# Optimization experiments

Hardware: AMD Instinct MI355X
Metric: run time of the kernel (lower is better)

## Reference

```python
import jax, jax.numpy as jnp
import numpy as np

IOU_POS = 0.5
IOU_NEG = 0.3


def _pairwise_iou(b1, b2):
    # b1: [N,4], b2: [M,4] in xyxy -> [N,M]
    area1 = (b1[:, 2] - b1[:, 0]) * (b1[:, 3] - b1[:, 1])
    area2 = (b2[:, 2] - b2[:, 0]) * (b2[:, 3] - b2[:, 1])
    lt = jnp.maximum(b1[:, None, :2], b2[None, :, :2])
    rb = jnp.minimum(b1[:, None, 2:], b2[None, :, 2:])
    wh = jnp.clip(rb - lt, 0.0)
    inter = wh[..., 0] * wh[..., 1]
    union = area1[:, None] + area2[None, :] - inter
    return inter / jnp.maximum(union, 1e-8)


def _smooth_l1(x):
    ax = jnp.abs(x)
    return jnp.where(ax < 1.0, 0.5 * x * x, ax - 0.5)


def _per_image(cls_o, reg_o, tb, tl):
    # cls_o: [N,C], reg_o: [N,4], tb: [M,4], tl: [M]
    ious = _pairwise_iou(reg_o, tb)            # [N,M]
    max_ious = ious.max(axis=1)
    max_idx = ious.argmax(axis=1)
    pos = max_ious >= IOU_POS
    neg = max_ious < IOU_NEG
    logp = jax.nn.log_softmax(cls_o, axis=-1)  # [N,C]
    matched_lbl = tl[max_idx]                  # [N]
    ce_pos = -jnp.take_along_axis(logp, matched_lbl[:, None], axis=1)[:, 0]
    ce_neg = -logp[:, 0]                       # background class 0
    npos = pos.sum().astype(logp.dtype)
    nneg = neg.sum().astype(logp.dtype)
    cls_loss_pos = jnp.sum(jnp.where(pos, ce_pos, 0.0)) / jnp.maximum(npos, 1.0)
    cls_loss_neg = jnp.sum(jnp.where(neg, ce_neg, 0.0)) / jnp.maximum(nneg, 1.0)
    diff = reg_o - tb[max_idx]                 # [N,4]
    sl1 = _smooth_l1(diff).mean(axis=-1)       # per-anchor mean over 4 coords
    reg_loss = jnp.sum(jnp.where(pos, sl1, 0.0)) / jnp.maximum(npos, 1.0)
    return cls_loss_pos, cls_loss_neg, reg_loss, npos > 0, nneg > 0


def _detection_loss(cls_output, reg_output, target_boxes, target_labels):
    cp, cn, rl, has_p, has_n = jax.vmap(_per_image)(cls_output, reg_output, target_boxes, target_labels)
    cls_vals = jnp.concatenate([cp, cn])
    cls_valid = jnp.concatenate([has_p, has_n]).astype(cls_vals.dtype)
    n_cls = cls_valid.sum()
    cls_mean = jnp.sum(cls_vals * cls_valid) / jnp.maximum(n_cls, 1.0)
    has_pf = has_p.astype(rl.dtype)
    n_reg = has_pf.sum()
    reg_mean = jnp.sum(rl * has_pf) / jnp.maximum(n_reg, 1.0)
    total = jnp.where(n_cls > 0, cls_mean, 0.0) + jnp.where(n_reg > 0, reg_mean, 0.0)
    return total


def setup_inputs() -> dict:
    key = jax.random.key(0)
    k1, k2, k3, k4, k5, k6 = jax.random.split(key, 6)
    B, N, C, M = 8, 131072, 21, 32
    cls_output = jax.random.normal(k1, (B, N, C), dtype=jnp.float32)
    xy = jax.random.uniform(k2, (B, N, 2), minval=0.0, maxval=220.0)
    wh = jax.random.uniform(k3, (B, N, 2), minval=20.0, maxval=80.0)
    reg_output = jnp.concatenate([xy, xy + wh], axis=-1)
    txy = jax.random.uniform(k4, (B, M, 2), minval=0.0, maxval=220.0)
    twh = jax.random.uniform(k5, (B, M, 2), minval=20.0, maxval=80.0)
    target_boxes = jnp.concatenate([txy, txy + twh], axis=-1)
    target_labels = jax.random.randint(k6, (B, M), 1, C)
    return {"cls_output": cls_output, "reg_output": reg_output,
            "target_boxes": target_boxes, "target_labels": target_labels}


def reference(cls_output, reg_output, target_boxes, target_labels):
    return _detection_loss(cls_output, reg_output, target_boxes, target_labels)
```

## Files before the change

### kernel.cpp

```cpp
#include <hip/hip_runtime.h>
#include <math.h>

#define TPB 256
#define TPB4 4
#define NC 21
#define NM 32

__global__ __launch_bounds__(TPB) void detloss_main(
    const float* __restrict__ cls, const float* __restrict__ reg,
    const float* __restrict__ tbx, const int* __restrict__ tlb,
    float* __restrict__ partials, int N, int gxb)
{
    __shared__ float s_red[TPB / 64][5];

    const int t    = threadIdx.x;
    const int lane = t & 63;
    const int w    = t >> 6;
    const int blk  = blockIdx.x;
    const int b    = blockIdx.y;
    const int ntiles = (N + TPB - 1) / TPB;
    const int tile0  = blk * TPB4;
    const int tile1  = min(tile0 + TPB4, ntiles);

    float v0 = 0.f, v1 = 0.f, v2 = 0.f, v3 = 0.f, v4 = 0.f;

    for (int tile = tile0; tile < tile1; ++tile) {
        const int row  = tile * TPB + t;
        const int rowi = (row < N) ? row : (N - 1);
        const float msk = (row < N) ? 1.f : 0.f;

        const float4 rg = ((const float4*)reg)[(size_t)b * N + rowi];
        const float a1 = (rg.z - rg.x) * (rg.w - rg.y);

        const char* xg = (const char*)(cls + ((size_t)b * N + rowi) * NC);
        float4 c0, c1, c2, c3, c4; float c5;
        __builtin_memcpy(&c0, xg,      16);
        __builtin_memcpy(&c1, xg + 16, 16);
        __builtin_memcpy(&c2, xg + 32, 16);
        __builtin_memcpy(&c3, xg + 48, 16);
        __builtin_memcpy(&c4, xg + 64, 16);
        __builtin_memcpy(&c5, xg + 80, 4);

        unsigned kbest = 0u;
        #pragma unroll
        for (int j = 0; j < NM; ++j) {
            const float4 tb = ((const float4*)tbx)[b * NM + j];
            const float ta = (tb.z - tb.x) * (tb.w - tb.y);
            const float lx = fmaxf(rg.x, tb.x), ly = fmaxf(rg.y, tb.y);
            const float rx = fminf(rg.z, tb.z), ry = fminf(rg.w, tb.w);
            const float wd = fmaxf(rx - lx, 0.f), h = fmaxf(ry - ly, 0.f);
            const float inter = wd * h;
            const float uni   = (a1 + ta) - inter;
            const float iou   = inter * __builtin_amdgcn_rcpf(uni);
            const unsigned key = (__float_as_uint(iou) & 0xFFFFFFE0u)
                               | (unsigned)(31 - j);
            kbest = (key > kbest) ? key : kbest;
        }
        const int   bidx = 31 - (int)(kbest & 31u);
        const float best = __uint_as_float(kbest & 0xFFFFFFE0u);
        const bool  pos  = (best >= 0.5f);
        const bool  neg  = (best <  0.3f);

        const int    lbl = tlb[b * NM + bidx];
        const float4 mb  = ((const float4*)tbx)[b * NM + bidx];
        float xlbl;
        __builtin_memcpy(&xlbl, xg + 4 * lbl, 4);

        float s0 = __expf(c0.x) + __expf(c0.y) + __expf(c0.z) + __expf(c0.w);
        float s1 = __expf(c1.x) + __expf(c1.y) + __expf(c1.z) + __expf(c1.w);
        float s2 = __expf(c2.x) + __expf(c2.y) + __expf(c2.z) + __expf(c2.w);
        float s3 = __expf(c3.x) + __expf(c3.y) + __expf(c3.z) + __expf(c3.w);
        s0 += __expf(c4.x) + __expf(c4.y);
        s1 += __expf(c4.z) + __expf(c4.w);
        s2 += __expf(c5);
        const float lse    = __logf((s0 + s1) + (s2 + s3));
        const float ce_pos = lse - xlbl;
        const float ce_neg = lse - c0.x;

        float sl = 0.f;
        {
            const float d0 = rg.x - mb.x, d1 = rg.y - mb.y;
            const float d2 = rg.z - mb.z, d3 = rg.w - mb.w;
            const float e0 = fabsf(d0), e1 = fabsf(d1);
            const float e2 = fabsf(d2), e3 = fabsf(d3);
            sl += (e0 < 1.f) ? 0.5f * d0 * d0 : (e0 - 0.5f);
            sl += (e1 < 1.f) ? 0.5f * d1 * d1 : (e1 - 0.5f);
            sl += (e2 < 1.f) ? 0.5f * d2 * d2 : (e2 - 0.5f);
            sl += (e3 < 1.f) ? 0.5f * d3 * d3 : (e3 - 0.5f);
            sl *= 0.25f;
        }

        const float pm = (pos ? 1.f : 0.f) * msk;
        const float nm = (neg ? 1.f : 0.f) * msk;
        v0 += pm * ce_pos; v2 += pm * sl; v3 += pm;
        v1 += nm * ce_neg; v4 += nm;
    }

    #pragma unroll
    for (int o = 32; o > 0; o >>= 1) {
        v0 += __shfl_down(v0, o);
        v1 += __shfl_down(v1, o);
        v2 += __shfl_down(v2, o);
        v3 += __shfl_down(v3, o);
        v4 += __shfl_down(v4, o);
    }
    if (lane == 0) {
        s_red[w][0] = v0; s_red[w][1] = v1; s_red[w][2] = v2;
        s_red[w][3] = v3; s_red[w][4] = v4;
    }
    __syncthreads();
    if (t == 0) {
        float r0 = 0, r1 = 0, r2 = 0, r3 = 0, r4 = 0;
        #pragma unroll
        for (int k = 0; k < TPB / 64; ++k) {
            r0 += s_red[k][0]; r1 += s_red[k][1]; r2 += s_red[k][2];
            r3 += s_red[k][3]; r4 += s_red[k][4];
        }
        float* q = partials + ((size_t)b * gxb + blk) * 5;
        q[0] = r0; q[1] = r1; q[2] = r2; q[3] = r3; q[4] = r4;
    }
}

__global__ __launch_bounds__(512) void detloss_final(
    const float* __restrict__ partials, int nblk, int B, float* __restrict__ out)
{
    __shared__ float s_img[8][5];
    const int t    = threadIdx.x;
    const int b    = t >> 6;
    const int lane = t & 63;

    if (b < B) {
        float v[5] = {0.f, 0.f, 0.f, 0.f, 0.f};
        for (int e = lane; e < nblk; e += 64) {
            const float* q = partials + ((size_t)b * nblk + e) * 5;
            #pragma unroll
            for (int k = 0; k < 5; ++k) v[k] += q[k];
        }
        #pragma unroll
        for (int o = 32; o > 0; o >>= 1) {
            #pragma unroll
            for (int k = 0; k < 5; ++k) v[k] += __shfl_down(v[k], o);
        }
        if (lane == 0) {
            const float npos = v[3], nneg = v[4];
            s_img[b][0] = v[0] / fmaxf(npos, 1.f);
            s_img[b][1] = v[1] / fmaxf(nneg, 1.f);
            s_img[b][2] = v[2] / fmaxf(npos, 1.f);
            s_img[b][3] = (npos > 0.f) ? 1.f : 0.f;
            s_img[b][4] = (nneg > 0.f) ? 1.f : 0.f;
        }
    }
    __syncthreads();

    if (t == 0) {
        float cls_sum = 0.f, n_cls = 0.f, reg_sum = 0.f, n_reg = 0.f;
        for (int b2 = 0; b2 < B; ++b2) {
            cls_sum += s_img[b2][0] * s_img[b2][3] + s_img[b2][1] * s_img[b2][4];
            n_cls   += s_img[b2][3] + s_img[b2][4];
            reg_sum += s_img[b2][2] * s_img[b2][3];
            n_reg   += s_img[b2][3];
        }
        const float cls_mean = cls_sum / fmaxf(n_cls, 1.f);
        const float reg_mean = reg_sum / fmaxf(n_reg, 1.f);
        out[0] = ((n_cls > 0.f) ? cls_mean : 0.f) + ((n_reg > 0.f) ? reg_mean : 0.f);
    }
}

extern "C" void kernel_launch(void* const* d_in, const int* in_sizes, int n_in,
                              void* d_out, int out_size, void* d_ws, size_t ws_size,
                              hipStream_t stream) {
    const float* cls = (const float*)d_in[0];
    const float* reg = (const float*)d_in[1];
    const float* tbx = (const float*)d_in[2];
    const int*   tlb = (const int*)d_in[3];
    float*       out = (float*)d_out;
    float*  partials = (float*)d_ws;

    const int B = 8;
    const int N = in_sizes[1] / (B * 4);
    const int ntiles = (N + TPB - 1) / TPB;
    const int gxb    = (ntiles + TPB4 - 1) / TPB4;

    dim3 grid(gxb, B);
    detloss_main<<<grid, TPB, 0, stream>>>(cls, reg, tbx, tlb, partials, N, gxb);
    detloss_final<<<1, 512, 0, stream>>>(partials, gxb, B, out);
}
```

Before: 40.74 us.

## Use one-wavefront blocks with one row per thread and no LDS reduction

The main kernel now launches 64-thread blocks, each thread handling exactly one anchor row. This replaces 256-thread blocks that looped over four tiles. The shared-memory cross-wave reduction and its barrier are removed, so each block writes its wavefront-reduced partials directly with a vector store. The aim is more independent loads in flight and less per-block synchronisation. In exchange the partials array grows 16-fold, and the single-block final kernel must sum many more strided entries.

```diff
diff --git a/kernel.cpp b/kernel.cpp
--- a/kernel.cpp
+++ b/kernel.cpp
@@ -1,100 +1,87 @@
 #include <hip/hip_runtime.h>
 #include <math.h>
 
-#define TPB 256
-#define TPB4 4
+#define WPB 64
 #define NC 21
 #define NM 32
 
-__global__ __launch_bounds__(TPB) void detloss_main(
+__global__ __launch_bounds__(WPB) void detloss_main(
     const float* __restrict__ cls, const float* __restrict__ reg,
     const float* __restrict__ tbx, const int* __restrict__ tlb,
-    float* __restrict__ partials, int N, int gxb)
+    float* __restrict__ partials, int N, int nblk)
 {
-    __shared__ float s_red[TPB / 64][5];
+    const int t   = threadIdx.x;
+    const int blk = blockIdx.x;
+    const int b   = blockIdx.y;
+    const int row = blk * WPB + t;
+    const int rowi = (row < N) ? row : (N - 1);
+    const float msk = (row < N) ? 1.f : 0.f;
 
-    const int t    = threadIdx.x;
-    const int lane = t & 63;
-    const int w    = t >> 6;
-    const int blk  = blockIdx.x;
-    const int b    = blockIdx.y;
-    const int ntiles = (N + TPB - 1) / TPB;
-    const int tile0  = blk * TPB4;
-    const int tile1  = min(tile0 + TPB4, ntiles);
+    const float4 rg = ((const float4*)reg)[(size_t)b * N + rowi];
+    const float a1 = (rg.z - rg.x) * (rg.w - rg.y);
 
-    float v0 = 0.f, v1 = 0.f, v2 = 0.f, v3 = 0.f, v4 = 0.f;
+    const char* xg = (const char*)(cls + ((size_t)b * N + rowi) * NC);
+    float4 c0, c1, c2, c3, c4; float c5;
+    __builtin_memcpy(&c0, xg,      16);
+    __builtin_memcpy(&c1, xg + 16, 16);
+    __builtin_memcpy(&c2, xg + 32, 16);
+    __builtin_memcpy(&c3, xg + 48, 16);
+    __builtin_memcpy(&c4, xg + 64, 16);
+    __builtin_memcpy(&c5, xg + 80, 4);
 
-    for (int tile = tile0; tile < tile1; ++tile) {
-        const int row  = tile * TPB + t;
-        const int rowi = (row < N) ? row : (N - 1);
-        const float msk = (row < N) ? 1.f : 0.f;
+    unsigned kbest = 0u;
+    #pragma unroll
+    for (int j = 0; j < NM; ++j) {
+        const float4 tb = ((const float4*)tbx)[b * NM + j];
+        const float ta = (tb.z - tb.x) * (tb.w - tb.y);
+        const float lx = fmaxf(rg.x, tb.x), ly = fmaxf(rg.y, tb.y);
+        const float rx = fminf(rg.z, tb.z), ry = fminf(rg.w, tb.w);
+        const float wd = fmaxf(rx - lx, 0.f), h = fmaxf(ry - ly, 0.f);
+        const float inter = wd * h;
+        const float uni   = (a1 + ta) - inter;
+        const float iou   = inter * __builtin_amdgcn_rcpf(uni);
+        const unsigned key = (__float_as_uint(iou) & 0xFFFFFFE0u)
+                           | (unsigned)(31 - j);
+        kbest = (key > kbest) ? key : kbest;
+    }
+    const int   bidx = 31 - (int)(kbest & 31u);
+    const float best = __uint_as_float(kbest & 0xFFFFFFE0u);
+    const bool  pos  = (best >= 0.5f);
+    const bool  neg  = (best <  0.3f);
 
-        const float4 rg = ((const float4*)reg)[(size_t)b * N + rowi];
-        const float a1 = (rg.z - rg.x) * (rg.w - rg.y);
+    const int    lbl = tlb[b * NM + bidx];
+    const float4 mb  = ((const float4*)tbx)[b * NM + bidx];
+    float xlbl;
+    __builtin_memcpy(&xlbl, xg + 4 * lbl, 4);
 
-        const char* xg = (const char*)(cls + ((size_t)b * N + rowi) * NC);
-        float4 c0, c1, c2, c3, c4; float c5;
-        __builtin_memcpy(&c0, xg,      16);
-        __builtin_memcpy(&c1, xg + 16, 16);
-        __builtin_memcpy(&c2, xg + 32, 16);
-        __builtin_memcpy(&c3, xg + 48, 16);
-        __builtin_memcpy(&c4, xg + 64, 16);
-        __builtin_memcpy(&c5, xg + 80, 4);
+    float s0 = __expf(c0.x) + __expf(c0.y) + __expf(c0.z) + __expf(c0.w);
+    float s1 = __expf(c1.x) + __expf(c1.y) + __expf(c1.z) + __expf(c1.w);
+    float s2 = __expf(c2.x) + __expf(c2.y) + __expf(c2.z) + __expf(c2.w);
+    float s3 = __expf(c3.x) + __expf(c3.y) + __expf(c3.z) + __expf(c3.w);
+    s0 += __expf(c4.x) + __expf(c4.y);
+    s1 += __expf(c4.z) + __expf(c4.w);
+    s2 += __expf(c5);
+    const float lse    = __logf((s0 + s1) + (s2 + s3));
+    const float ce_pos = lse - xlbl;
+    const float ce_neg = lse - c0.x;
 
-        unsigned kbest = 0u;
-        #pragma unroll
-        for (int j = 0; j < NM; ++j) {
-            const float4 tb = ((const float4*)tbx)[b * NM + j];
-            const float ta = (tb.z - tb.x) * (tb.w - tb.y);
-            const float lx = fmaxf(rg.x, tb.x), ly = fmaxf(rg.y, tb.y);
-            const float rx = fminf(rg.z, tb.z), ry = fminf(rg.w, tb.w);
-            const float wd = fmaxf(rx - lx, 0.f), h = fmaxf(ry - ly, 0.f);
-            const float inter = wd * h;
-            const float uni   = (a1 + ta) - inter;
-            const float iou   = inter * __builtin_amdgcn_rcpf(uni);
-            const unsigned key = (__float_as_uint(iou) & 0xFFFFFFE0u)
-                               | (unsigned)(31 - j);
-            kbest = (key > kbest) ? key : kbest;
-        }
-        const int   bidx = 31 - (int)(kbest & 31u);
-        const float best = __uint_as_float(kbest & 0xFFFFFFE0u);
-        const bool  pos  = (best >= 0.5f);
-        const bool  neg  = (best <  0.3f);
+    float sl = 0.f;
+    {
+        const float d0 = rg.x - mb.x, d1 = rg.y - mb.y;
+        const float d2 = rg.z - mb.z, d3 = rg.w - mb.w;
+        const float e0 = fabsf(d0), e1 = fabsf(d1);
+        const float e2 = fabsf(d2), e3 = fabsf(d3);
+        sl += (e0 < 1.f) ? 0.5f * d0 * d0 : (e0 - 0.5f);
+        sl += (e1 < 1.f) ? 0.5f * d1 * d1 : (e1 - 0.5f);
+        sl += (e2 < 1.f) ? 0.5f * d2 * d2 : (e2 - 0.5f);
+        sl += (e3 < 1.f) ? 0.5f * d3 * d3 : (e3 - 0.5f);
+        sl *= 0.25f;
+    }
 
-        const int    lbl = tlb[b * NM + bidx];
-        const float4 mb  = ((const float4*)tbx)[b * NM + bidx];
-        float xlbl;
-        __builtin_memcpy(&xlbl, xg + 4 * lbl, 4);
-
-        float s0 = __expf(c0.x) + __expf(c0.y) + __expf(c0.z) + __expf(c0.w);
-        float s1 = __expf(c1.x) + __expf(c1.y) + __expf(c1.z) + __expf(c1.w);
-        float s2 = __expf(c2.x) + __expf(c2.y) + __expf(c2.z) + __expf(c2.w);
-        float s3 = __expf(c3.x) + __expf(c3.y) + __expf(c3.z) + __expf(c3.w);
-        s0 += __expf(c4.x) + __expf(c4.y);
-        s1 += __expf(c4.z) + __expf(c4.w);
-        s2 += __expf(c5);
-        const float lse    = __logf((s0 + s1) + (s2 + s3));
-        const float ce_pos = lse - xlbl;
-        const float ce_neg = lse - c0.x;
-
-        float sl = 0.f;
-        {
-            const float d0 = rg.x - mb.x, d1 = rg.y - mb.y;
-            const float d2 = rg.z - mb.z, d3 = rg.w - mb.w;
-            const float e0 = fabsf(d0), e1 = fabsf(d1);
-            const float e2 = fabsf(d2), e3 = fabsf(d3);
-            sl += (e0 < 1.f) ? 0.5f * d0 * d0 : (e0 - 0.5f);
-            sl += (e1 < 1.f) ? 0.5f * d1 * d1 : (e1 - 0.5f);
-            sl += (e2 < 1.f) ? 0.5f * d2 * d2 : (e2 - 0.5f);
-            sl += (e3 < 1.f) ? 0.5f * d3 * d3 : (e3 - 0.5f);
-            sl *= 0.25f;
-        }
-
-        const float pm = (pos ? 1.f : 0.f) * msk;
-        const float nm = (neg ? 1.f : 0.f) * msk;
-        v0 += pm * ce_pos; v2 += pm * sl; v3 += pm;
-        v1 += nm * ce_neg; v4 += nm;
-    }
+    const float pm = (pos ? 1.f : 0.f) * msk;
+    const float nm = (neg ? 1.f : 0.f) * msk;
+    float v0 = pm * ce_pos, v2 = pm * sl, v3 = pm;
+    float v1 = nm * ce_neg, v4 = nm;
 
     #pragma unroll
     for (int o = 32; o > 0; o >>= 1) {
@@ -104,20 +91,11 @@
         v3 += __shfl_down(v3, o);
         v4 += __shfl_down(v4, o);
     }
-    if (lane == 0) {
-        s_red[w][0] = v0; s_red[w][1] = v1; s_red[w][2] = v2;
-        s_red[w][3] = v3; s_red[w][4] = v4;
-    }
-    __syncthreads();
     if (t == 0) {
-        float r0 = 0, r1 = 0, r2 = 0, r3 = 0, r4 = 0;
-        #pragma unroll
-        for (int k = 0; k < TPB / 64; ++k) {
-            r0 += s_red[k][0]; r1 += s_red[k][1]; r2 += s_red[k][2];
-            r3 += s_red[k][3]; r4 += s_red[k][4];
-        }
-        float* q = partials + ((size_t)b * gxb + blk) * 5;
-        q[0] = r0; q[1] = r1; q[2] = r2; q[3] = r3; q[4] = r4;
+        float* q = partials + ((size_t)b * nblk + blk) * 5;
+        float4 p4 = make_float4(v0, v1, v2, v3);
+        __builtin_memcpy(q, &p4, 16);
+        q[4] = v4;
     }
 }
 
@@ -133,8 +111,10 @@
         float v[5] = {0.f, 0.f, 0.f, 0.f, 0.f};
         for (int e = lane; e < nblk; e += 64) {
             const float* q = partials + ((size_t)b * nblk + e) * 5;
-            #pragma unroll
-            for (int k = 0; k < 5; ++k) v[k] += q[k];
+            float4 p4; float p5;
+            __builtin_memcpy(&p4, q, 16);
+            p5 = q[4];
+            v[0] += p4.x; v[1] += p4.y; v[2] += p4.z; v[3] += p4.w; v[4] += p5;
         }
         #pragma unroll
         for (int o = 32; o > 0; o >>= 1) {
@@ -178,10 +158,9 @@
 
     const int B = 8;
     const int N = in_sizes[1] / (B * 4);
-    const int ntiles = (N + TPB - 1) / TPB;
-    const int gxb    = (ntiles + TPB4 - 1) / TPB4;
+    const int nblk = (N + WPB - 1) / WPB;
 
-    dim3 grid(gxb, B);
-    detloss_main<<<grid, TPB, 0, stream>>>(cls, reg, tbx, tlb, partials, N, gxb);
-    detloss_final<<<1, 512, 0, stream>>>(partials, gxb, B, out);
+    dim3 grid(nblk, B);
+    detloss_main<<<grid, WPB, 0, stream>>>(cls, reg, tbx, tlb, partials, N, nblk);
+    detloss_final<<<1, 512, 0, stream>>>(partials, nblk, B, out);
 }
```

Measured after the change: 39.82 us. 2.3% less time.

## Fuse final reduction into main kernel via last-block atomic counter

Applied to the files above, without the earlier changes.

The separate finalize kernel is removed. Each block now publishes its partials, then increments a global counter, and the last block to finish performs the cross-block and cross-image reduction. The per-block tile loop is also dropped, so each block handles one 256-row tile and the grid grows fourfold. This trades one kernel launch for a memset and an atomic per block. The final reduction now reads four times as many partials, and every block pays extra launch overhead.

```diff
diff --git a/kernel.cpp b/kernel.cpp
--- a/kernel.cpp
+++ b/kernel.cpp
@@ -2,99 +2,93 @@
 #include <math.h>
 
 #define TPB 256
-#define TPB4 4
 #define NC 21
 #define NM 32
 
 __global__ __launch_bounds__(TPB) void detloss_main(
     const float* __restrict__ cls, const float* __restrict__ reg,
     const float* __restrict__ tbx, const int* __restrict__ tlb,
-    float* __restrict__ partials, int N, int gxb)
+    float* __restrict__ partials, unsigned* __restrict__ counter,
+    float* __restrict__ out, int N, int nblk, int B)
 {
     __shared__ float s_red[TPB / 64][5];
+    __shared__ float s_img[8][5];
+    __shared__ int   s_last;
 
     const int t    = threadIdx.x;
     const int lane = t & 63;
     const int w    = t >> 6;
     const int blk  = blockIdx.x;
     const int b    = blockIdx.y;
-    const int ntiles = (N + TPB - 1) / TPB;
-    const int tile0  = blk * TPB4;
-    const int tile1  = min(tile0 + TPB4, ntiles);
+    const int row  = blk * TPB + t;
+    const int rowi = (row < N) ? row : (N - 1);
+    const float msk = (row < N) ? 1.f : 0.f;
 
-    float v0 = 0.f, v1 = 0.f, v2 = 0.f, v3 = 0.f, v4 = 0.f;
+    const float4 rg = ((const float4*)reg)[(size_t)b * N + rowi];
+    const float a1 = (rg.z - rg.x) * (rg.w - rg.y);
 
-    for (int tile = tile0; tile < tile1; ++tile) {
-        const int row  = tile * TPB + t;
-        const int rowi = (row < N) ? row : (N - 1);
-        const float msk = (row < N) ? 1.f : 0.f;
+    const char* xg = (const char*)(cls + ((size_t)b * N + rowi) * NC);
+    float4 c0, c1, c2, c3, c4; float c5;
+    __builtin_memcpy(&c0, xg,      16);
+    __builtin_memcpy(&c1, xg + 16, 16);
+    __builtin_memcpy(&c2, xg + 32, 16);
+    __builtin_memcpy(&c3, xg + 48, 16);
+    __builtin_memcpy(&c4, xg + 64, 16);
+    __builtin_memcpy(&c5, xg + 80, 4);
 
-        const float4 rg = ((const float4*)reg)[(size_t)b * N + rowi];
-        const float a1 = (rg.z - rg.x) * (rg.w - rg.y);
+    unsigned kbest = 0u;
+    #pragma unroll
+    for (int j = 0; j < NM; ++j) {
+        const float4 tb = ((const float4*)tbx)[b * NM + j];
+        const float ta = (tb.z - tb.x) * (tb.w - tb.y);
+        const float lx = fmaxf(rg.x, tb.x), ly = fmaxf(rg.y, tb.y);
+        const float rx = fminf(rg.z, tb.z), ry = fminf(rg.w, tb.w);
+        const float wd = fmaxf(rx - lx, 0.f), h = fmaxf(ry - ly, 0.f);
+        const float inter = wd * h;
+        const float uni   = (a1 + ta) - inter;
+        const float iou   = inter * __builtin_amdgcn_rcpf(uni);
+        const unsigned key = (__float_as_uint(iou) & 0xFFFFFFE0u)
+                           | (unsigned)(31 - j);
+        kbest = (key > kbest) ? key : kbest;
+    }
+    const int   bidx = 31 - (int)(kbest & 31u);
+    const float best = __uint_as_float(kbest & 0xFFFFFFE0u);
+    const bool  pos  = (best >= 0.5f);
+    const bool  neg  = (best <  0.3f);
 
-        const char* xg = (const char*)(cls + ((size_t)b * N + rowi) * NC);
-        float4 c0, c1, c2, c3, c4; float c5;
-        __builtin_memcpy(&c0, xg,      16);
-        __builtin_memcpy(&c1, xg + 16, 16);
-        __builtin_memcpy(&c2, xg + 32, 16);
-        __builtin_memcpy(&c3, xg + 48, 16);
-        __builtin_memcpy(&c4, xg + 64, 16);
-        __builtin_memcpy(&c5, xg + 80, 4);
+    const int    lbl = tlb[b * NM + bidx];
+    const float4 mb  = ((const float4*)tbx)[b * NM + bidx];
+    float xlbl;
+    __builtin_memcpy(&xlbl, xg + 4 * lbl, 4);
 
-        unsigned kbest = 0u;
-        #pragma unroll
-        for (int j = 0; j < NM; ++j) {
-            const float4 tb = ((const float4*)tbx)[b * NM + j];
-            const float ta = (tb.z - tb.x) * (tb.w - tb.y);
-            const float lx = fmaxf(rg.x, tb.x), ly = fmaxf(rg.y, tb.y);
-            const float rx = fminf(rg.z, tb.z), ry = fminf(rg.w, tb.w);
-            const float wd = fmaxf(rx - lx, 0.f), h = fmaxf(ry - ly, 0.f);
-            const float inter = wd * h;
-            const float uni   = (a1 + ta) - inter;
-            const float iou   = inter * __builtin_amdgcn_rcpf(uni);
-            const unsigned key = (__float_as_uint(iou) & 0xFFFFFFE0u)
-                               | (unsigned)(31 - j);
-            kbest = (key > kbest) ? key : kbest;
-        }
-        const int   bidx = 31 - (int)(kbest & 31u);
-        const float best = __uint_as_float(kbest & 0xFFFFFFE0u);
-        const bool  pos  = (best >= 0.5f);
-        const bool  neg  = (best <  0.3f);
+    float s0 = __expf(c0.x) + __expf(c0.y) + __expf(c0.z) + __expf(c0.w);
+    float s1 = __expf(c1.x) + __expf(c1.y) + __expf(c1.z) + __expf(c1.w);
+    float s2 = __expf(c2.x) + __expf(c2.y) + __expf(c2.z) + __expf(c2.w);
+    float s3 = __expf(c3.x) + __expf(c3.y) + __expf(c3.z) + __expf(c3.w);
+    s0 += __expf(c4.x) + __expf(c4.y);
+    s1 += __expf(c4.z) + __expf(c4.w);
+    s2 += __expf(c5);
+    const float lse    = __logf((s0 + s1) + (s2 + s3));
+    const float ce_pos = lse - xlbl;
+    const float ce_neg = lse - c0.x;
 
-        const int    lbl = tlb[b * NM + bidx];
-        const float4 mb  = ((const float4*)tbx)[b * NM + bidx];
-        float xlbl;
-        __builtin_memcpy(&xlbl, xg + 4 * lbl, 4);
+    float sl = 0.f;
+    {
+        const float d0 = rg.x - mb.x, d1 = rg.y - mb.y;
+        const float d2 = rg.z - mb.z, d3 = rg.w - mb.w;
+        const float e0 = fabsf(d0), e1 = fabsf(d1);
+        const float e2 = fabsf(d2), e3 = fabsf(d3);
+        sl += (e0 < 1.f) ? 0.5f * d0 * d0 : (e0 - 0.5f);
+        sl += (e1 < 1.f) ? 0.5f * d1 * d1 : (e1 - 0.5f);
+        sl += (e2 < 1.f) ? 0.5f * d2 * d2 : (e2 - 0.5f);
+        sl += (e3 < 1.f) ? 0.5f * d3 * d3 : (e3 - 0.5f);
+        sl *= 0.25f;
+    }
 
-        float s0 = __expf(c0.x) + __expf(c0.y) + __expf(c0.z) + __expf(c0.w);
-        float s1 = __expf(c1.x) + __expf(c1.y) + __expf(c1.z) + __expf(c1.w);
-        float s2 = __expf(c2.x) + __expf(c2.y) + __expf(c2.z) + __expf(c2.w);
-        float s3 = __expf(c3.x) + __expf(c3.y) + __expf(c3.z) + __expf(c3.w);
-        s0 += __expf(c4.x) + __expf(c4.y);
-        s1 += __expf(c4.z) + __expf(c4.w);
-        s2 += __expf(c5);
-        const float lse    = __logf((s0 + s1) + (s2 + s3));
-        const float ce_pos = lse - xlbl;
-        const float ce_neg = lse - c0.x;
-
-        float sl = 0.f;
-        {
-            const float d0 = rg.x - mb.x, d1 = rg.y - mb.y;
-            const float d2 = rg.z - mb.z, d3 = rg.w - mb.w;
-            const float e0 = fabsf(d0), e1 = fabsf(d1);
-            const float e2 = fabsf(d2), e3 = fabsf(d3);
-            sl += (e0 < 1.f) ? 0.5f * d0 * d0 : (e0 - 0.5f);
-            sl += (e1 < 1.f) ? 0.5f * d1 * d1 : (e1 - 0.5f);
-            sl += (e2 < 1.f) ? 0.5f * d2 * d2 : (e2 - 0.5f);
-            sl += (e3 < 1.f) ? 0.5f * d3 * d3 : (e3 - 0.5f);
-            sl *= 0.25f;
-        }
-
-        const float pm = (pos ? 1.f : 0.f) * msk;
-        const float nm = (neg ? 1.f : 0.f) * msk;
-        v0 += pm * ce_pos; v2 += pm * sl; v3 += pm;
-        v1 += nm * ce_neg; v4 += nm;
-    }
+    const float pm = (pos ? 1.f : 0.f) * msk;
+    const float nm = (neg ? 1.f : 0.f) * msk;
+    float v0 = pm * ce_pos, v2 = pm * sl, v3 = pm;
+    float v1 = nm * ce_neg, v4 = nm;
 
     #pragma unroll
     for (int o = 32; o > 0; o >>= 1) {
@@ -116,42 +110,43 @@
             r0 += s_red[k][0]; r1 += s_red[k][1]; r2 += s_red[k][2];
             r3 += s_red[k][3]; r4 += s_red[k][4];
         }
-        float* q = partials + ((size_t)b * gxb + blk) * 5;
+        float* q = partials + ((size_t)b * nblk + blk) * 5;
         q[0] = r0; q[1] = r1; q[2] = r2; q[3] = r3; q[4] = r4;
+        __threadfence();
+        const unsigned old = atomicAdd(counter, 1u);
+        s_last = (old == (unsigned)(nblk * B) - 1u) ? 1 : 0;
     }
-}
+    __syncthreads();
+    if (s_last == 0) return;
 
-__global__ __launch_bounds__(512) void detloss_final(
-    const float* __restrict__ partials, int nblk, int B, float* __restrict__ out)
-{
-    __shared__ float s_img[8][5];
-    const int t    = threadIdx.x;
-    const int b    = t >> 6;
-    const int lane = t & 63;
-
-    if (b < B) {
-        float v[5] = {0.f, 0.f, 0.f, 0.f, 0.f};
+    __threadfence();
+    #pragma unroll
+    for (int half = 0; half < 2; ++half) {
+        const int bb = w + 4 * half;
+        float u0 = 0.f, u1 = 0.f, u2 = 0.f, u3 = 0.f, u4 = 0.f;
         for (int e = lane; e < nblk; e += 64) {
-            const float* q = partials + ((size_t)b * nblk + e) * 5;
-            #pragma unroll
-            for (int k = 0; k < 5; ++k) v[k] += q[k];
+            const float* q = partials + ((size_t)bb * nblk + e) * 5;
+            float4 p4; __builtin_memcpy(&p4, q, 16);
+            u0 += p4.x; u1 += p4.y; u2 += p4.z; u3 += p4.w; u4 += q[4];
         }
         #pragma unroll
         for (int o = 32; o > 0; o >>= 1) {
-            #pragma unroll
-            for (int k = 0; k < 5; ++k) v[k] += __shfl_down(v[k], o);
+            u0 += __shfl_down(u0, o);
+            u1 += __shfl_down(u1, o);
+            u2 += __shfl_down(u2, o);
+            u3 += __shfl_down(u3, o);
+            u4 += __shfl_down(u4, o);
         }
         if (lane == 0) {
-            const float npos = v[3], nneg = v[4];
-            s_img[b][0] = v[0] / fmaxf(npos, 1.f);
-            s_img[b][1] = v[1] / fmaxf(nneg, 1.f);
-            s_img[b][2] = v[2] / fmaxf(npos, 1.f);
-            s_img[b][3] = (npos > 0.f) ? 1.f : 0.f;
-            s_img[b][4] = (nneg > 0.f) ? 1.f : 0.f;
+            const float npos = u3, nneg = u4;
+            s_img[bb][0] = u0 / fmaxf(npos, 1.f);
+            s_img[bb][1] = u1 / fmaxf(nneg, 1.f);
+            s_img[bb][2] = u2 / fmaxf(npos, 1.f);
+            s_img[bb][3] = (npos > 0.f) ? 1.f : 0.f;
+            s_img[bb][4] = (nneg > 0.f) ? 1.f : 0.f;
         }
     }
     __syncthreads();
-
     if (t == 0) {
         float cls_sum = 0.f, n_cls = 0.f, reg_sum = 0.f, n_reg = 0.f;
         for (int b2 = 0; b2 < B; ++b2) {
@@ -174,14 +169,17 @@
     const float* tbx = (const float*)d_in[2];
     const int*   tlb = (const int*)d_in[3];
     float*       out = (float*)d_out;
-    float*  partials = (float*)d_ws;
+
+    char* ws = (char*)d_ws;
+    unsigned* counter  = (unsigned*)ws;
+    float*    partials = (float*)(ws + 256);
 
     const int B = 8;
     const int N = in_sizes[1] / (B * 4);
-    const int ntiles = (N + TPB - 1) / TPB;
-    const int gxb    = (ntiles + TPB4 - 1) / TPB4;
+    const int nblk = (N + TPB - 1) / TPB;
 
-    dim3 grid(gxb, B);
-    detloss_main<<<grid, TPB, 0, stream>>>(cls, reg, tbx, tlb, partials, N, gxb);
-    detloss_final<<<1, 512, 0, stream>>>(partials, gxb, B, out);
+    hipMemsetAsync(counter, 0, sizeof(unsigned), stream);
+    dim3 grid(nblk, B);
+    detloss_main<<<grid, TPB, 0, stream>>>(cls, reg, tbx, tlb, partials,
+                                           counter, out, N, nblk, B);
 }
```

Measured after the change: 156.2 us. +283.3%, slower.
